# Kernel optimization log

Measured on AMD Instinct MI355X. Metric: run time of the kernel, lower is better.

The kernel has to match this reference:

```python
import jax, jax.numpy as jnp
import numpy as np

NUM_LINKS = 1048576


def _euler_rots(theta):
    # theta: [N,3] -> per-link rotation R = Rz @ Ry @ Rx, shape [N,3,3]
    cx, cy, cz = jnp.cos(theta[:, 0]), jnp.cos(theta[:, 1]), jnp.cos(theta[:, 2])
    sx, sy, sz = jnp.sin(theta[:, 0]), jnp.sin(theta[:, 1]), jnp.sin(theta[:, 2])
    z = jnp.zeros_like(cx)
    o = jnp.ones_like(cx)
    rx = jnp.stack([jnp.stack([o, z, z], -1),
                    jnp.stack([z, cx, -sx], -1),
                    jnp.stack([z, sx, cx], -1)], -2)
    ry = jnp.stack([jnp.stack([cy, z, sy], -1),
                    jnp.stack([z, o, z], -1),
                    jnp.stack([-sy, z, cy], -1)], -2)
    rz = jnp.stack([jnp.stack([cz, -sz, z], -1),
                    jnp.stack([sz, cz, z], -1),
                    jnp.stack([z, z, o], -1)], -2)
    return jnp.matmul(rz, jnp.matmul(ry, rx))  # [N,3,3]


def setup_inputs() -> dict:
    key = jax.random.key(0)
    k1, k2 = jax.random.split(key)
    link_lengths = jax.random.uniform(k1, (NUM_LINKS,), dtype=jnp.float32)
    theta = jax.random.normal(k2, (NUM_LINKS, 3), dtype=jnp.float32)
    return {"link_lengths": link_lengths, "theta": theta}


def reference(link_lengths, theta):
    # Original loop computes eff_pos_i = sum_{j=0..i} (R_0 @ R_1 @ ... @ R_j) @ t_j
    # with t_j = l_j * e_z. Vectorize via prefix matrix products + cumsum.
    R = _euler_rots(theta)                                   # [N,3,3]
    P = jax.lax.associative_scan(jnp.matmul, R)              # P_j = R_0@...@R_j
    v = P[:, :, 2] * link_lengths[:, None]                   # P_j @ (l_j * e_z)
    return jnp.cumsum(v, axis=0)                             # [N,3]
```

## Files before the change

### kernel.cpp

```cpp
#include <hip/hip_runtime.h>
#include <math.h>


#define K1_TPB 512
#define K1_EPT 2
#define K1_EPB (K1_TPB * K1_EPT)
#define K1_NW (K1_TPB / 64)
#define K3_TPB 256
#define K3_EPT 4
#define K3_EPB (K3_TPB * K3_EPT)
#define MAXB 1024
#define EPG (MAXB / 256)

struct Xf {
    float m[9];
    float p[3];
};

__device__ __forceinline__ void xf_identity(Xf& x) {
    x.m[0] = 1.f; x.m[1] = 0.f; x.m[2] = 0.f;
    x.m[3] = 0.f; x.m[4] = 1.f; x.m[5] = 0.f;
    x.m[6] = 0.f; x.m[7] = 0.f; x.m[8] = 1.f;
    x.p[0] = 0.f; x.p[1] = 0.f; x.p[2] = 0.f;
}

__device__ __forceinline__ Xf xf_comb(const Xf& A, const Xf& B) {
    Xf o;
#pragma unroll
    for (int r = 0; r < 3; ++r) {
        const float a0 = A.m[r * 3 + 0], a1 = A.m[r * 3 + 1], a2 = A.m[r * 3 + 2];
#pragma unroll
        for (int c = 0; c < 3; ++c) {
            o.m[r * 3 + c] = a0 * B.m[0 * 3 + c] + a1 * B.m[1 * 3 + c] + a2 * B.m[2 * 3 + c];
        }
        o.p[r] = A.p[r] + a0 * B.p[0] + a1 * B.p[1] + a2 * B.p[2];
    }
    return o;
}

__device__ __forceinline__ void fast_sincos(float x, float& s, float& c) {
    const float fn = __builtin_rintf(x * 0.636619772367581343f);
    const int n = (int)fn;
    float r = __builtin_fmaf(fn, -1.57079637050628662109375f, x);
    r = __builtin_fmaf(fn, 4.37113900018624283e-8f, r);
    const float r2 = r * r;
    float sp = __builtin_fmaf(r2, -1.9515295891e-4f, 8.3321608736e-3f);
    sp = __builtin_fmaf(r2, sp, -1.6666654611e-1f);
    const float ss = __builtin_fmaf(r * r2, sp, r);
    float cp = __builtin_fmaf(r2, 2.443315711809948e-5f, -1.388731625493765e-3f);
    cp = __builtin_fmaf(r2, cp, 4.166664568298827e-2f);
    const float cc = __builtin_fmaf(r2 * r2, cp,
                                    __builtin_fmaf(r2, -0.5f, 1.0f));
    const int q = n & 3;
    const float s0 = (q & 1) ? cc : ss;
    const float c0 = (q & 1) ? ss : cc;
    const unsigned sgn_s = (unsigned)(q & 2) << 30;
    const unsigned sgn_c = (unsigned)((q + 1) & 2) << 30;
    s = __uint_as_float(__float_as_uint(s0) ^ sgn_s);
    c = __uint_as_float(__float_as_uint(c0) ^ sgn_c);
}

__device__ __forceinline__ void xf_fold(Xf& a, float ax, float ay, float az, float l) {
    float sx, cx, sy, cy, sz, cz;
    fast_sincos(ax, sx, cx);
    fast_sincos(ay, sy, cy);
    fast_sincos(az, sz, cz);
    const float sysx = sy * sx, sycx = sy * cx;
    const float r00 = cz * cy;
    const float r01 = cz * sysx - sz * cx;
    const float r02 = sz * sx + cz * sycx;
    const float r10 = sz * cy;
    const float r11 = cz * cx + sz * sysx;
    const float r12 = sz * sycx - cz * sx;
    const float r20 = -sy;
    const float r21 = cy * sx;
    const float r22 = cy * cx;
    const float t0 = l * r02, t1 = l * r12, t2 = l * r22;
    const float p0 = a.p[0] + a.m[0] * t0 + a.m[1] * t1 + a.m[2] * t2;
    const float p1 = a.p[1] + a.m[3] * t0 + a.m[4] * t1 + a.m[5] * t2;
    const float p2 = a.p[2] + a.m[6] * t0 + a.m[7] * t1 + a.m[8] * t2;
    const float n0 = a.m[0] * r00 + a.m[1] * r10 + a.m[2] * r20;
    const float n1 = a.m[0] * r01 + a.m[1] * r11 + a.m[2] * r21;
    const float n2 = a.m[0] * r02 + a.m[1] * r12 + a.m[2] * r22;
    const float n3 = a.m[3] * r00 + a.m[4] * r10 + a.m[5] * r20;
    const float n4 = a.m[3] * r01 + a.m[4] * r11 + a.m[5] * r21;
    const float n5 = a.m[3] * r02 + a.m[4] * r12 + a.m[5] * r22;
    const float n6 = a.m[6] * r00 + a.m[7] * r10 + a.m[8] * r20;
    const float n7 = a.m[6] * r01 + a.m[7] * r11 + a.m[8] * r21;
    const float n8 = a.m[6] * r02 + a.m[7] * r12 + a.m[8] * r22;
    a.m[0] = n0; a.m[1] = n1; a.m[2] = n2;
    a.m[3] = n3; a.m[4] = n4; a.m[5] = n5;
    a.m[6] = n6; a.m[7] = n7; a.m[8] = n8;
    a.p[0] = p0; a.p[1] = p1; a.p[2] = p2;
}

template <int CTRL, int RMASK>
__device__ __forceinline__ float dpp_f(float src, float oldv) {
    return __int_as_float(__builtin_amdgcn_update_dpp(
        __float_as_int(oldv), __float_as_int(src), CTRL, RMASK, 0xF, false));
}

template <int CTRL, int RMASK>
__device__ __forceinline__ Xf xf_scan_step(const Xf& v) {
    Xf b;
    b.m[0] = dpp_f<CTRL, RMASK>(v.m[0], 1.f);
    b.m[1] = dpp_f<CTRL, RMASK>(v.m[1], 0.f);
    b.m[2] = dpp_f<CTRL, RMASK>(v.m[2], 0.f);
    b.m[3] = dpp_f<CTRL, RMASK>(v.m[3], 0.f);
    b.m[4] = dpp_f<CTRL, RMASK>(v.m[4], 1.f);
    b.m[5] = dpp_f<CTRL, RMASK>(v.m[5], 0.f);
    b.m[6] = dpp_f<CTRL, RMASK>(v.m[6], 0.f);
    b.m[7] = dpp_f<CTRL, RMASK>(v.m[7], 0.f);
    b.m[8] = dpp_f<CTRL, RMASK>(v.m[8], 1.f);
    b.p[0] = dpp_f<CTRL, RMASK>(v.p[0], 0.f);
    b.p[1] = dpp_f<CTRL, RMASK>(v.p[1], 0.f);
    b.p[2] = dpp_f<CTRL, RMASK>(v.p[2], 0.f);
    return xf_comb(b, v);
}

__device__ __forceinline__ Xf wave_scan(Xf v) {
    v = xf_scan_step<0x111, 0xF>(v);
    v = xf_scan_step<0x112, 0xF>(v);
    v = xf_scan_step<0x114, 0xF>(v);
    v = xf_scan_step<0x118, 0xF>(v);
    v = xf_scan_step<0x142, 0xA>(v);
    v = xf_scan_step<0x143, 0xC>(v);
    return v;
}

__device__ __forceinline__ Xf xf_shfl_up1(const Xf& a) {
    Xf o;
#pragma unroll
    for (int k = 0; k < 9; ++k) o.m[k] = __shfl_up(a.m[k], 1, 64);
#pragma unroll
    for (int k = 0; k < 3; ++k) o.p[k] = __shfl_up(a.p[k], 1, 64);
    return o;
}

__device__ __forceinline__ Xf xf_load4(const Xf* p) {
    const float4* g = (const float4*)p;
    const float4 x = g[0], y = g[1], z = g[2];
    Xf b;
    b.m[0] = x.x; b.m[1] = x.y; b.m[2] = x.z;
    b.m[3] = x.w; b.m[4] = y.x; b.m[5] = y.y;
    b.m[6] = y.z; b.m[7] = y.w; b.m[8] = z.x;
    b.p[0] = z.y; b.p[1] = z.z; b.p[2] = z.w;
    return b;
}
__device__ __forceinline__ void xf_store4(Xf* p, const Xf& b) {
    float4* g = (float4*)p;
    g[0] = make_float4(b.m[0], b.m[1], b.m[2], b.m[3]);
    g[1] = make_float4(b.m[4], b.m[5], b.m[6], b.m[7]);
    g[2] = make_float4(b.m[8], b.p[0], b.p[1], b.p[2]);
}

__device__ __forceinline__ void xf_apply(const Xf& T, float q0, float q1, float q2,
                                         float& o0, float& o1, float& o2) {
    o0 = T.p[0] + T.m[0] * q0 + T.m[1] * q1 + T.m[2] * q2;
    o1 = T.p[1] + T.m[3] * q0 + T.m[4] * q1 + T.m[5] * q2;
    o2 = T.p[2] + T.m[6] * q0 + T.m[7] * q1 + T.m[8] * q2;
}

__global__ void __launch_bounds__(K1_TPB, 8)
fk_local(const float* __restrict__ ll, const float* __restrict__ th,
         Xf* __restrict__ agg, float* __restrict__ out, int n) {
    __shared__ Xf wagg[K1_NW];
    const int t = threadIdx.x, bid = blockIdx.x;
    const int lane = t & 63, w = t >> 6;
    const long long j0 = (long long)bid * K1_EPB + (long long)t * K1_EPT;

    Xf a;
    xf_identity(a);
    float pe[K1_EPT][3];
    if (j0 + K1_EPT <= n) {
        const float2* th2 = (const float2*)(th + 3 * j0);
        const float2 d0 = th2[0], d1 = th2[1], d2 = th2[2];
        const float2 L = *(const float2*)(ll + j0);
        xf_fold(a, d0.x, d0.y, d1.x, L.x);
        pe[0][0] = a.p[0]; pe[0][1] = a.p[1]; pe[0][2] = a.p[2];
        xf_fold(a, d1.y, d2.x, d2.y, L.y);
        pe[1][0] = a.p[0]; pe[1][1] = a.p[1]; pe[1][2] = a.p[2];
    } else {
#pragma unroll
        for (int e = 0; e < K1_EPT; ++e) {
            const long long j = j0 + e;
            if (j < n) xf_fold(a, th[3 * j + 0], th[3 * j + 1], th[3 * j + 2], ll[j]);
            pe[e][0] = a.p[0]; pe[e][1] = a.p[1]; pe[e][2] = a.p[2];
        }
    }

    const Xf inc = wave_scan(a);
    if (lane == 63) wagg[w] = inc;
    __syncthreads();

    Xf exw;
    xf_identity(exw);
    for (int k = 0; k < w; ++k) exw = xf_comb(exw, wagg[k]);

    if (t == K1_TPB - 1) xf_store4(&agg[bid], xf_comb(exw, inc));

    const Xf ext = xf_shfl_up1(inc);
    Xf T = exw;
    if (lane != 0) T = xf_comb(T, ext);

    if (j0 + K1_EPT <= n) {
        float o0, o1, o2, o3, o4, o5;
        xf_apply(T, pe[0][0], pe[0][1], pe[0][2], o0, o1, o2);
        xf_apply(T, pe[1][0], pe[1][1], pe[1][2], o3, o4, o5);
        float2* q2 = (float2*)(out + 3 * j0);
        q2[0] = make_float2(o0, o1);
        q2[1] = make_float2(o2, o3);
        q2[2] = make_float2(o4, o5);
    } else {
#pragma unroll
        for (int e = 0; e < K1_EPT; ++e) {
            const long long j = j0 + e;
            if (j < n) {
                float o0, o1, o2;
                xf_apply(T, pe[e][0], pe[e][1], pe[e][2], o0, o1, o2);
                out[3 * j + 0] = o0; out[3 * j + 1] = o1; out[3 * j + 2] = o2;
            }
        }
    }
}

__global__ void __launch_bounds__(256)
fk_scanagg(const Xf* __restrict__ agg, Xf* __restrict__ pfx, int nb) {
    __shared__ Xf wagg[4];
    const int t = threadIdx.x;
    const int lane = t & 63, w = t >> 6;
    const int i0 = t * EPG;

    Xf q[EPG];
    Xf a;
    xf_identity(a);
#pragma unroll
    for (int e = 0; e < EPG; ++e) {
        const int i = i0 + e;
        if (i < nb) a = xf_comb(a, xf_load4(&agg[i]));
        q[e] = a;
    }

    const Xf inc = wave_scan(a);
    if (lane == 63) wagg[w] = inc;
    __syncthreads();

    Xf exw;
    xf_identity(exw);
    for (int k = 0; k < w; ++k) exw = xf_comb(exw, wagg[k]);

    const Xf ext = xf_shfl_up1(inc);
    Xf T = exw;
    if (lane != 0) T = xf_comb(T, ext);

    if (i0 < nb) xf_store4(&pfx[i0], T);
#pragma unroll
    for (int e = 1; e < EPG; ++e) {
        if (i0 + e < nb) {
            Xf v = xf_comb(T, q[e - 1]);
            xf_store4(&pfx[i0 + e], v);
        }
    }
}

__global__ void __launch_bounds__(K3_TPB, 8)
fk_fixup(const Xf* __restrict__ pfx, float* __restrict__ out, int n) {
    const int t = threadIdx.x, bid = blockIdx.x;
    const Xf G = xf_load4(&pfx[bid]);

    const long long j0 = (long long)bid * K3_EPB + (long long)t * K3_EPT;
    if (j0 + K3_EPT <= n) {
        float4* o4 = (float4*)(out + 3 * j0);
        const float4 x = o4[0], y = o4[1], z = o4[2];
        float r[12];
        xf_apply(G, x.x, x.y, x.z, r[0], r[1], r[2]);
        xf_apply(G, x.w, y.x, y.y, r[3], r[4], r[5]);
        xf_apply(G, y.z, y.w, z.x, r[6], r[7], r[8]);
        xf_apply(G, z.y, z.z, z.w, r[9], r[10], r[11]);
        o4[0] = make_float4(r[0], r[1], r[2], r[3]);
        o4[1] = make_float4(r[4], r[5], r[6], r[7]);
        o4[2] = make_float4(r[8], r[9], r[10], r[11]);
    } else {
#pragma unroll
        for (int e = 0; e < K3_EPT; ++e) {
            const long long j = j0 + e;
            if (j < n) {
                float o0, o1, o2;
                xf_apply(G, out[3 * j + 0], out[3 * j + 1], out[3 * j + 2], o0, o1, o2);
                out[3 * j + 0] = o0; out[3 * j + 1] = o1; out[3 * j + 2] = o2;
            }
        }
    }
}

extern "C" void kernel_launch(void* const* d_in, const int* in_sizes, int n_in,
                              void* d_out, int out_size, void* d_ws, size_t ws_size,
                              hipStream_t stream) {
    const float* ll = (const float*)d_in[0];
    const float* th = (const float*)d_in[1];
    float* out = (float*)d_out;
    const int n = in_sizes[0];

    int nb = (n + K1_EPB - 1) / K1_EPB;
    if (nb > MAXB) nb = MAXB;

    Xf* agg = (Xf*)d_ws;
    Xf* pfx = agg + MAXB;

    fk_local<<<nb, K1_TPB, 0, stream>>>(ll, th, agg, out, n);
    fk_scanagg<<<1, 256, 0, stream>>>(agg, pfx, nb);
    fk_fixup<<<nb, K3_TPB, 0, stream>>>(pfx, out, n);
}
```

Before: 36.16 us.

## Fold block-aggregate scan into fixup kernel, removing single-block scan launch

Removes the separate single-block kernel that scanned the per-block aggregates. Each fixup block now reduces all aggregates before its own index to get its prefix transform, then applies it. This drops one kernel launch and its serial dependency. In exchange every block redundantly reads and combines up to 1024 aggregates, and two extra block barriers are added before the output update.

```diff
diff --git a/kernel.cpp b/kernel.cpp
--- a/kernel.cpp
+++ b/kernel.cpp
@@ -6,11 +6,12 @@
 #define K1_EPT 2
 #define K1_EPB (K1_TPB * K1_EPT)
 #define K1_NW (K1_TPB / 64)
-#define K3_TPB 256
-#define K3_EPT 4
-#define K3_EPB (K3_TPB * K3_EPT)
+#define K2_TPB 256
+#define K2_EPT 4
+#define K2_EPB (K2_TPB * K2_EPT)
+#define K2_NW (K2_TPB / 64)
 #define MAXB 1024
-#define EPG (MAXB / 256)
+#define EPG (MAXB / K2_TPB)
 
 struct Xf {
     float m[9];
@@ -224,52 +225,37 @@
     }
 }
 
-__global__ void __launch_bounds__(256)
-fk_scanagg(const Xf* __restrict__ agg, Xf* __restrict__ pfx, int nb) {
-    __shared__ Xf wagg[4];
-    const int t = threadIdx.x;
+__global__ void __launch_bounds__(K2_TPB, 8)
+fk_fixup(const Xf* __restrict__ agg, float* __restrict__ out, int n, int nb) {
+    __shared__ Xf wred[K2_NW];
+    __shared__ Xf shG;
+    const int t = threadIdx.x, bid = blockIdx.x;
     const int lane = t & 63, w = t >> 6;
-    const int i0 = t * EPG;
-
-    Xf q[EPG];
-    Xf a;
-    xf_identity(a);
-#pragma unroll
-    for (int e = 0; e < EPG; ++e) {
-        const int i = i0 + e;
-        if (i < nb) a = xf_comb(a, xf_load4(&agg[i]));
-        q[e] = a;
-    }
-
-    const Xf inc = wave_scan(a);
-    if (lane == 63) wagg[w] = inc;
+
+    {
+        const int i0 = t * EPG;
+        Xf A;
+        xf_identity(A);
+#pragma unroll
+        for (int e = 0; e < EPG; ++e) {
+            const int i = i0 + e;
+            if (i < bid) A = xf_comb(A, xf_load4(&agg[i]));
+        }
+        const Xf inc = wave_scan(A);
+        if (lane == 63) wred[w] = inc;
+    }
     __syncthreads();
-
-    Xf exw;
-    xf_identity(exw);
-    for (int k = 0; k < w; ++k) exw = xf_comb(exw, wagg[k]);
-
-    const Xf ext = xf_shfl_up1(inc);
-    Xf T = exw;
-    if (lane != 0) T = xf_comb(T, ext);
-
-    if (i0 < nb) xf_store4(&pfx[i0], T);
-#pragma unroll
-    for (int e = 1; e < EPG; ++e) {
-        if (i0 + e < nb) {
-            Xf v = xf_comb(T, q[e - 1]);
-            xf_store4(&pfx[i0 + e], v);
-        }
-    }
-}
-
-__global__ void __launch_bounds__(K3_TPB, 8)
-fk_fixup(const Xf* __restrict__ pfx, float* __restrict__ out, int n) {
-    const int t = threadIdx.x, bid = blockIdx.x;
-    const Xf G = xf_load4(&pfx[bid]);
-
-    const long long j0 = (long long)bid * K3_EPB + (long long)t * K3_EPT;
-    if (j0 + K3_EPT <= n) {
+    if (t == 0) {
+        Xf G = wred[0];
+#pragma unroll
+        for (int k = 1; k < K2_NW; ++k) G = xf_comb(G, wred[k]);
+        shG = G;
+    }
+    __syncthreads();
+    const Xf G = shG;
+
+    const long long j0 = (long long)bid * K2_EPB + (long long)t * K2_EPT;
+    if (j0 + K2_EPT <= n) {
         float4* o4 = (float4*)(out + 3 * j0);
         const float4 x = o4[0], y = o4[1], z = o4[2];
         float r[12];
@@ -282,7 +268,7 @@
         o4[2] = make_float4(r[8], r[9], r[10], r[11]);
     } else {
 #pragma unroll
-        for (int e = 0; e < K3_EPT; ++e) {
+        for (int e = 0; e < K2_EPT; ++e) {
             const long long j = j0 + e;
             if (j < n) {
                 float o0, o1, o2;
@@ -305,9 +291,7 @@
     if (nb > MAXB) nb = MAXB;
 
     Xf* agg = (Xf*)d_ws;
-    Xf* pfx = agg + MAXB;
 
     fk_local<<<nb, K1_TPB, 0, stream>>>(ll, th, agg, out, n);
-    fk_scanagg<<<1, 256, 0, stream>>>(agg, pfx, nb);
-    fk_fixup<<<nb, K3_TPB, 0, stream>>>(pfx, out, n);
-}
+    fk_fixup<<<nb, K2_TPB, 0, stream>>>(agg, out, n, nb);
+}
```

New measurement: 33.01 us. -8.7%, faster.
